# Kernel tuning notes

Hardware: AMD Instinct MI355X
Metric: run time of the kernel (lower is better)

Reference implementation:

```python
import jax, jax.numpy as jnp
import numpy as np

B, L, D = 4, 2048, 256
MAX_NGRAM = 3
SLOTS = 64


def setup_inputs() -> dict:
    key = jax.random.key(0)
    k1, k2, k3 = jax.random.split(key, 3)
    x = jax.random.normal(k1, (B, L, D), dtype=jnp.float32)
    memory = jax.random.normal(k2, (SLOTS, MAX_NGRAM, D), dtype=jnp.float32)
    pos_bias = jax.random.normal(k3, (SLOTS, MAX_NGRAM), dtype=jnp.float32)
    return {"x": x, "memory": memory, "pos_bias": pos_bias}


def _extract_ngrams(x, max_ngram):
    # Left-pad with max_ngram-1 zero vectors, then take max_ngram shifted views.
    b, l, d = x.shape
    xpad = jnp.concatenate([jnp.zeros((b, max_ngram - 1, d), x.dtype), x], axis=1)
    # ngrams[b, l, n] = xpad[b, n + l]  -> (B, L, N, d)
    return jnp.stack([xpad[:, n:n + l] for n in range(max_ngram)], axis=2)


def reference(x, memory, pos_bias):
    slots, max_ngram, d = memory.shape
    ngrams = _extract_ngrams(x, max_ngram)                      # (B, L, N, d)
    # Contraction over d replaces the huge (B,L,M,N,d) broadcast-multiply.
    sims = jnp.einsum('blnd,mnd->blmn', ngrams, memory)         # (B, L, M, N)
    scores = sims + pos_bias[None, None]                        # (B, L, M, N)
    best = jnp.argmax(scores, axis=-1)                          # (B, L, M) int
    # selected[b,l,m] = memory[m, best[b,l,m]]  -> (B, L, M, d)
    selected = memory[jnp.arange(slots)[None, None, :], best]
    return selected.sum(axis=2)                                 # (B, L, d)
```

## Files before the change

kernel.cpp:

```cpp
#include <hip/hip_runtime.h>
#include <stdint.h>

#define LL   2048
#define DD   256
#define SLOTS 64
#define MN   192
#define PT   8192

typedef _Float16 half8 __attribute__((ext_vector_type(8)));
typedef float    f32x4 __attribute__((ext_vector_type(4)));

#define FRAG_ELEMS (MN * DD)

__global__ __launch_bounds__(256) void prep_kernel(
    const float* __restrict__ mem,
    _Float16* __restrict__ aS_h, _Float16* __restrict__ aS_l,
    _Float16* __restrict__ bG_h)
{
    const int e = blockIdx.x * 256 + threadIdx.x;
    const int mn = e >> 8;
    const int d  = e & 255;
    const float v = mem[e];
    const _Float16 h  = (_Float16)v;
    const _Float16 lo = (_Float16)(v - (float)h);

    {
        const int tm = mn >> 4, r = mn & 15;
        const int c = d >> 5, q = (d >> 3) & 3, j = d & 7;
        const int i1 = ((tm * 8 + c) * 64 + (q * 16 + r)) * 8 + j;
        aS_h[i1] = h; aS_l[i1] = lo;
    }
    {
        const int c2 = mn >> 5, q2 = (mn >> 3) & 3, j2 = mn & 7;
        const int td = d >> 4, n2 = d & 15;
        const int i2 = ((td * 6 + c2) * 64 + (q2 * 16 + n2)) * 8 + j2;
        bG_h[i2] = h;
    }
}

__global__ __launch_bounds__(256) void fused_kernel(
    const float* __restrict__ x, const float* __restrict__ bias,
    const _Float16* __restrict__ aS_h, const _Float16* __restrict__ aS_l,
    const _Float16* __restrict__ bG_h,
    float* __restrict__ out)
{
    __shared__ _Float16 xfh[2 * 8 * 64 * 8];
    __shared__ _Float16 xfl[2 * 8 * 64 * 8];
    __shared__ float    scores[MN * 18];
    __shared__ float    biasS[MN];
    __shared__ uint32_t selS[16 * 8];

    const int p0   = blockIdx.x * 16;
    const int tid  = threadIdx.x;
    const int lane = tid & 63;
    const int w    = tid >> 6;
    const int q    = lane >> 4, col = lane & 15;

    half8 ah[2][3], al[2][3];
#pragma unroll
    for (int i = 0; i < 3; ++i) {
        const int tm = w * 3 + i;
        const size_t off = (size_t)((tm * 8 + 0) * 64 + lane) * 8;
        ah[0][i] = *(const half8*)(aS_h + off);
        al[0][i] = *(const half8*)(aS_l + off);
    }

    if (tid < 128) selS[tid] = 0u;
    if (tid < MN)  biasS[tid] = bias[tid];

    {
        const int c  = tid & 7;
        const int rr = tid >> 3;
        int g = p0 - 2 + rr;
        g = g < 0 ? 0 : (g > PT - 1 ? PT - 1 : g);
        const float4* xr = (const float4*)(x + (size_t)g * DD + c * 32);
        const int pt = rr >> 4, lr = rr & 15;
#pragma unroll
        for (int qq = 0; qq < 4; ++qq) {
            const float4 u = xr[qq * 2];
            const float4 v = xr[qq * 2 + 1];
            float f[8] = {u.x, u.y, u.z, u.w, v.x, v.y, v.z, v.w};
            half8 hi, lo;
#pragma unroll
            for (int j = 0; j < 8; ++j) {
                const _Float16 h = (_Float16)f[j];
                hi[j] = h;
                lo[j] = (_Float16)(f[j] - (float)h);
            }
            const int base = ((pt * 8 + c) * 64 + qq * 16 + lr) * 8;
            *(half8*)(xfh + base) = hi;
            *(half8*)(xfl + base) = lo;
        }
    }
    __syncthreads();

    {
        f32x4 acc[3][2];
#pragma unroll
        for (int i = 0; i < 3; ++i)
#pragma unroll
            for (int p = 0; p < 2; ++p) acc[i][p] = (f32x4){0.f, 0.f, 0.f, 0.f};

        half8 bh[2][2], bl[2][2];
#pragma unroll
        for (int p = 0; p < 2; ++p) {
            const int base = ((p * 8 + 0) * 64 + lane) * 8;
            bh[0][p] = *(const half8*)(xfh + base);
            bl[0][p] = *(const half8*)(xfl + base);
        }

#pragma unroll
        for (int c = 0; c < 8; ++c) {
            const int cur = c & 1, nxt = cur ^ 1;
            if (c < 7) {
#pragma unroll
                for (int i = 0; i < 3; ++i) {
                    const int tm = w * 3 + i;
                    const size_t off = (size_t)((tm * 8 + c + 1) * 64 + lane) * 8;
                    ah[nxt][i] = *(const half8*)(aS_h + off);
                    al[nxt][i] = *(const half8*)(aS_l + off);
                }
#pragma unroll
                for (int p = 0; p < 2; ++p) {
                    const int base = ((p * 8 + c + 1) * 64 + lane) * 8;
                    bh[nxt][p] = *(const half8*)(xfh + base);
                    bl[nxt][p] = *(const half8*)(xfl + base);
                }
            }
#pragma unroll
            for (int i = 0; i < 3; ++i)
#pragma unroll
                for (int p = 0; p < 2; ++p) {
                    acc[i][p] = __builtin_amdgcn_mfma_f32_16x16x32_f16(ah[cur][i], bh[cur][p], acc[i][p], 0, 0, 0);
                    acc[i][p] = __builtin_amdgcn_mfma_f32_16x16x32_f16(ah[cur][i], bl[cur][p], acc[i][p], 0, 0, 0);
                    acc[i][p] = __builtin_amdgcn_mfma_f32_16x16x32_f16(al[cur][i], bh[cur][p], acc[i][p], 0, 0, 0);
                }
        }

#pragma unroll
        for (int i = 0; i < 3; ++i) {
            const int tm = w * 3 + i;
#pragma unroll
            for (int p = 0; p < 2; ++p) {
                const int wp = p * 16 + col;
                if (wp < 18) {
#pragma unroll
                    for (int r = 0; r < 4; ++r)
                        scores[(tm * 16 + q * 4 + r) * 18 + wp] = acc[i][p][r];
                }
            }
        }
    }

    half8 mg[2][4];
#pragma unroll
    for (int i = 0; i < 4; ++i) {
        const int td = w * 4 + i;
        const size_t off = (size_t)((td * 6 + 0) * 64 + lane) * 8;
        mg[0][i] = *(const half8*)(bG_h + off);
    }
    __syncthreads();

#pragma unroll
    for (int it = 0; it < 4; ++it) {
        const int t2 = tid + it * 256;
        const int pl = t2 & 15;
        const int m  = t2 >> 4;
        const int p  = p0 + pl;
        const int l  = p & (LL - 1);
        const float v0 = ((l >= 2) ? scores[(3 * m + 0) * 18 + pl + 0] : 0.f) + biasS[3 * m + 0];
        const float v1 = ((l >= 1) ? scores[(3 * m + 1) * 18 + pl + 1] : 0.f) + biasS[3 * m + 1];
        const float v2 =              scores[(3 * m + 2) * 18 + pl + 2]       + biasS[3 * m + 2];
        int bn = 0; float bv = v0;
        if (v1 > bv) { bv = v1; bn = 1; }
        if (v2 > bv) { bv = v2; bn = 2; }
        const int mnb = 3 * m + bn;
        atomicOr(&selS[pl * 8 + (mnb >> 5)], 1u << (mnb & 31));
    }
    __syncthreads();

    {
        uint32_t sw[6];
#pragma unroll
        for (int c = 0; c < 6; ++c) sw[c] = selS[col * 8 + c];

        f32x4 acc2[4];
#pragma unroll
        for (int i = 0; i < 4; ++i) acc2[i] = (f32x4){0.f, 0.f, 0.f, 0.f};

        const _Float16 ONE = (_Float16)1.f, ZERO = (_Float16)0.f;
        const int qb = q * 8;
#pragma unroll
        for (int c = 0; c < 6; ++c) {
            const int cur = c & 1, nxt = cur ^ 1;
            if (c < 5) {
#pragma unroll
                for (int i = 0; i < 4; ++i) {
                    const int td = w * 4 + i;
                    const size_t off = (size_t)((td * 6 + c + 1) * 64 + lane) * 8;
                    mg[nxt][i] = *(const half8*)(bG_h + off);
                }
            }
            half8 sel;
#pragma unroll
            for (int j = 0; j < 8; ++j)
                sel[j] = ((sw[c] >> (qb + j)) & 1u) ? ONE : ZERO;
#pragma unroll
            for (int i = 0; i < 4; ++i)
                acc2[i] = __builtin_amdgcn_mfma_f32_16x16x32_f16(sel, mg[cur][i], acc2[i], 0, 0, 0);
        }

#pragma unroll
        for (int i = 0; i < 4; ++i) {
            const int td = w * 4 + i;
#pragma unroll
            for (int r = 0; r < 4; ++r)
                out[(size_t)(p0 + q * 4 + r) * DD + td * 16 + col] = acc2[i][r];
        }
    }
}

extern "C" void kernel_launch(void* const* d_in, const int* in_sizes, int n_in,
                              void* d_out, int out_size, void* d_ws, size_t ws_size,
                              hipStream_t stream) {
    (void)in_sizes; (void)n_in; (void)out_size; (void)ws_size;
    const float* x    = (const float*)d_in[0];
    const float* mem  = (const float*)d_in[1];
    const float* bias = (const float*)d_in[2];
    float* out = (float*)d_out;

    _Float16* aS_h = (_Float16*)d_ws;
    _Float16* aS_l = aS_h + FRAG_ELEMS;
    _Float16* bG_h = aS_l + FRAG_ELEMS;

    prep_kernel<<<FRAG_ELEMS / 256, 256, 0, stream>>>(mem, aS_h, aS_l, bG_h);
    fused_kernel<<<PT / 16, 256, 0, stream>>>(x, bias, aS_h, aS_l, bG_h, out);
}
```

Baseline: 76.25 us.

## Fold memory-bank fp16 split into main kernel, drop prep launch

Removes the separate prep kernel that converted the memory bank into pre-swizzled fp16 hi/lo fragment buffers in workspace. The main kernel now loads fp32 memory rows directly from global memory and does the hi/lo split in registers before each MFMA. The gather stage loads strided fp32 columns and converts them on the fly. This saves a kernel launch and the workspace round-trip, but every block now redoes the conversion and the gather loads are strided and uncoalesced.

```diff
diff --git a/kernel.cpp b/kernel.cpp
--- a/kernel.cpp
+++ b/kernel.cpp
@@ -3,46 +3,15 @@
 
 #define LL   2048
 #define DD   256
-#define SLOTS 64
 #define MN   192
 #define PT   8192
 
 typedef _Float16 half8 __attribute__((ext_vector_type(8)));
 typedef float    f32x4 __attribute__((ext_vector_type(4)));
 
-#define FRAG_ELEMS (MN * DD)
-
-__global__ __launch_bounds__(256) void prep_kernel(
-    const float* __restrict__ mem,
-    _Float16* __restrict__ aS_h, _Float16* __restrict__ aS_l,
-    _Float16* __restrict__ bG_h)
-{
-    const int e = blockIdx.x * 256 + threadIdx.x;
-    const int mn = e >> 8;
-    const int d  = e & 255;
-    const float v = mem[e];
-    const _Float16 h  = (_Float16)v;
-    const _Float16 lo = (_Float16)(v - (float)h);
-
-    {
-        const int tm = mn >> 4, r = mn & 15;
-        const int c = d >> 5, q = (d >> 3) & 3, j = d & 7;
-        const int i1 = ((tm * 8 + c) * 64 + (q * 16 + r)) * 8 + j;
-        aS_h[i1] = h; aS_l[i1] = lo;
-    }
-    {
-        const int c2 = mn >> 5, q2 = (mn >> 3) & 3, j2 = mn & 7;
-        const int td = d >> 4, n2 = d & 15;
-        const int i2 = ((td * 6 + c2) * 64 + (q2 * 16 + n2)) * 8 + j2;
-        bG_h[i2] = h;
-    }
-}
-
 __global__ __launch_bounds__(256) void fused_kernel(
-    const float* __restrict__ x, const float* __restrict__ bias,
-    const _Float16* __restrict__ aS_h, const _Float16* __restrict__ aS_l,
-    const _Float16* __restrict__ bG_h,
-    float* __restrict__ out)
+    const float* __restrict__ x, const float* __restrict__ mem,
+    const float* __restrict__ bias, float* __restrict__ out)
 {
     __shared__ _Float16 xfh[2 * 8 * 64 * 8];
     __shared__ _Float16 xfl[2 * 8 * 64 * 8];
@@ -56,13 +25,16 @@
     const int w    = tid >> 6;
     const int q    = lane >> 4, col = lane & 15;
 
-    half8 ah[2][3], al[2][3];
+    const float* aB[3];
+#pragma unroll
+    for (int i = 0; i < 3; ++i)
+        aB[i] = mem + (size_t)((w * 3 + i) * 16 + col) * DD + q * 8;
+
+    float4 au[2][3][2];
 #pragma unroll
     for (int i = 0; i < 3; ++i) {
-        const int tm = w * 3 + i;
-        const size_t off = (size_t)((tm * 8 + 0) * 64 + lane) * 8;
-        ah[0][i] = *(const half8*)(aS_h + off);
-        al[0][i] = *(const half8*)(aS_l + off);
+        au[0][i][0] = *(const float4*)(aB[i]);
+        au[0][i][1] = *(const float4*)(aB[i] + 4);
     }
 
     if (tid < 128) selS[tid] = 0u;
@@ -115,10 +87,8 @@
             if (c < 7) {
 #pragma unroll
                 for (int i = 0; i < 3; ++i) {
-                    const int tm = w * 3 + i;
-                    const size_t off = (size_t)((tm * 8 + c + 1) * 64 + lane) * 8;
-                    ah[nxt][i] = *(const half8*)(aS_h + off);
-                    al[nxt][i] = *(const half8*)(aS_l + off);
+                    au[nxt][i][0] = *(const float4*)(aB[i] + (c + 1) * 32);
+                    au[nxt][i][1] = *(const float4*)(aB[i] + (c + 1) * 32 + 4);
                 }
 #pragma unroll
                 for (int p = 0; p < 2; ++p) {
@@ -127,13 +97,24 @@
                     bl[nxt][p] = *(const half8*)(xfl + base);
                 }
             }
+            half8 ah[3], al[3];
+#pragma unroll
+            for (int i = 0; i < 3; ++i) {
+                const float* fp = (const float*)&au[cur][i][0];
+#pragma unroll
+                for (int j = 0; j < 8; ++j) {
+                    const _Float16 h = (_Float16)fp[j];
+                    ah[i][j] = h;
+                    al[i][j] = (_Float16)(fp[j] - (float)h);
+                }
+            }
 #pragma unroll
             for (int i = 0; i < 3; ++i)
 #pragma unroll
                 for (int p = 0; p < 2; ++p) {
-                    acc[i][p] = __builtin_amdgcn_mfma_f32_16x16x32_f16(ah[cur][i], bh[cur][p], acc[i][p], 0, 0, 0);
-                    acc[i][p] = __builtin_amdgcn_mfma_f32_16x16x32_f16(ah[cur][i], bl[cur][p], acc[i][p], 0, 0, 0);
-                    acc[i][p] = __builtin_amdgcn_mfma_f32_16x16x32_f16(al[cur][i], bh[cur][p], acc[i][p], 0, 0, 0);
+                    acc[i][p] = __builtin_amdgcn_mfma_f32_16x16x32_f16(ah[i], bh[cur][p], acc[i][p], 0, 0, 0);
+                    acc[i][p] = __builtin_amdgcn_mfma_f32_16x16x32_f16(ah[i], bl[cur][p], acc[i][p], 0, 0, 0);
+                    acc[i][p] = __builtin_amdgcn_mfma_f32_16x16x32_f16(al[i], bh[cur][p], acc[i][p], 0, 0, 0);
                 }
         }
 
@@ -152,13 +133,13 @@
         }
     }
 
-    half8 mg[2][4];
-#pragma unroll
-    for (int i = 0; i < 4; ++i) {
-        const int td = w * 4 + i;
-        const size_t off = (size_t)((td * 6 + 0) * 64 + lane) * 8;
-        mg[0][i] = *(const half8*)(bG_h + off);
-    }
+    const float* dB = mem + (size_t)(q * 8) * DD + col;
+    float colv[2][4][8];
+#pragma unroll
+    for (int i = 0; i < 4; ++i)
+#pragma unroll
+        for (int j = 0; j < 8; ++j)
+            colv[0][i][j] = dB[(size_t)j * DD + (w * 4 + i) * 16];
     __syncthreads();
 
 #pragma unroll
@@ -195,19 +176,22 @@
             const int cur = c & 1, nxt = cur ^ 1;
             if (c < 5) {
 #pragma unroll
-                for (int i = 0; i < 4; ++i) {
-                    const int td = w * 4 + i;
-                    const size_t off = (size_t)((td * 6 + c + 1) * 64 + lane) * 8;
-                    mg[nxt][i] = *(const half8*)(bG_h + off);
-                }
+                for (int i = 0; i < 4; ++i)
+#pragma unroll
+                    for (int j = 0; j < 8; ++j)
+                        colv[nxt][i][j] = dB[(size_t)((c + 1) * 32 + j) * DD + (w * 4 + i) * 16];
             }
             half8 sel;
 #pragma unroll
             for (int j = 0; j < 8; ++j)
                 sel[j] = ((sw[c] >> (qb + j)) & 1u) ? ONE : ZERO;
 #pragma unroll
-            for (int i = 0; i < 4; ++i)
-                acc2[i] = __builtin_amdgcn_mfma_f32_16x16x32_f16(sel, mg[cur][i], acc2[i], 0, 0, 0);
+            for (int i = 0; i < 4; ++i) {
+                half8 bf;
+#pragma unroll
+                for (int j = 0; j < 8; ++j) bf[j] = (_Float16)colv[cur][i][j];
+                acc2[i] = __builtin_amdgcn_mfma_f32_16x16x32_f16(sel, bf, acc2[i], 0, 0, 0);
+            }
         }
 
 #pragma unroll
@@ -223,16 +207,11 @@
 extern "C" void kernel_launch(void* const* d_in, const int* in_sizes, int n_in,
                               void* d_out, int out_size, void* d_ws, size_t ws_size,
                               hipStream_t stream) {
-    (void)in_sizes; (void)n_in; (void)out_size; (void)ws_size;
+    (void)in_sizes; (void)n_in; (void)out_size; (void)d_ws; (void)ws_size;
     const float* x    = (const float*)d_in[0];
     const float* mem  = (const float*)d_in[1];
     const float* bias = (const float*)d_in[2];
     float* out = (float*)d_out;
 
-    _Float16* aS_h = (_Float16*)d_ws;
-    _Float16* aS_l = aS_h + FRAG_ELEMS;
-    _Float16* bG_h = aS_l + FRAG_ELEMS;
-
-    prep_kernel<<<FRAG_ELEMS / 256, 256, 0, stream>>>(mem, aS_h, aS_l, bG_h);
-    fused_kernel<<<PT / 16, 256, 0, stream>>>(x, bias, aS_h, aS_l, bG_h, out);
+    fused_kernel<<<PT / 16, 256, 0, stream>>>(x, mem, bias, out);
 }
```

After: 80.69 us. 1.06x slower.
